# Kernel optimization log

Hardware: AMD Instinct MI355X
Metric: run time of the kernel (lower is better)

The kernel has to match this reference:

```python
import jax, jax.numpy as jnp
import numpy as np

TEMPERATURE = 0.1
B, D, A = 8192, 256, 4


def setup_inputs() -> dict:
    key = jax.random.key(0)
    k1, k2 = jax.random.split(key)
    # scale by 1/sqrt(D) so dot products are O(1) and exp(sim/T) is finite
    embeddings = jax.random.normal(k1, (B, D), dtype=jnp.float32) / jnp.sqrt(jnp.float32(D))
    labels = jax.random.randint(k2, (B, A), 0, 6, dtype=jnp.int64)
    return {"embeddings": embeddings, "labels": labels}


def reference(embeddings, labels):
    b = embeddings.shape[0]
    # [B, B] similarity scaled by temperature
    sim = jnp.matmul(embeddings, embeddings.T) / TEMPERATURE
    # positive mask: ANY aspect matches (vectorized over aspects), diagonal zeroed
    pos_mask = jnp.any(labels[:, None, :] == labels[None, :, :], axis=-1)
    pos_mask = pos_mask & ~jnp.eye(b, dtype=bool)
    pos_mask = pos_mask.astype(sim.dtype)

    exp_sim = jnp.exp(sim)
    positive_sim = jnp.sum(exp_sim * pos_mask, axis=1)            # [B]
    all_sim = jnp.sum(exp_sim, axis=1) - jnp.diagonal(exp_sim)   # [B]

    valid = positive_sim > 0
    pos_safe = jnp.where(valid, positive_sim, 1.0)
    all_safe = jnp.where(valid, all_sim, 1.0)
    row_loss = jnp.where(valid, -jnp.log(pos_safe / (all_safe + 1e-8)), 0.0)

    num_pos = jnp.sum(valid.astype(sim.dtype))
    loss = jnp.where(num_pos > 0, jnp.sum(row_loss) / jnp.maximum(num_pos, 1.0), 0.0)
    return loss
```

## Files before the change

### kernel.cpp

```cpp
#include <hip/hip_runtime.h>
#include <stdint.h>

typedef float f32x4 __attribute__((ext_vector_type(4)));
typedef float f32x2 __attribute__((ext_vector_type(2)));
typedef long lng2 __attribute__((ext_vector_type(2)));

#define B_TOTAL 8192
#define DDIM 256
#define BM 128
#define BN 64
#define NSPLIT 16
#define COLS_PER (B_TOTAL / NSPLIT)
#define ITERS (COLS_PER / BN)
#define NBLOCKS ((B_TOTAL / BM) * NSPLIT)
#define SCALE_HALF 3.79828546f
#define LN2F 0.6931471805599453f

__global__ __launch_bounds__(256) void prep_all(
    const float* __restrict__ E, const int* __restrict__ lab,
    unsigned char* __restrict__ EbA, unsigned char* __restrict__ Bf,
    unsigned int* __restrict__ plab, float* __restrict__ posAll) {
  const int t = blockIdx.x * 256 + threadIdx.x;
  const float4* s4 = (const float4*)E + (size_t)t * 2;
  float4 v0 = s4[0], v1 = s4[1];
  unsigned int d0 = (unsigned int)__builtin_amdgcn_cvt_pk_fp8_f32(
      v0.x * SCALE_HALF, v0.y * SCALE_HALF, 0, false);
  d0 = (unsigned int)__builtin_amdgcn_cvt_pk_fp8_f32(
      v0.z * SCALE_HALF, v0.w * SCALE_HALF, (int)d0, true);
  unsigned int d1 = (unsigned int)__builtin_amdgcn_cvt_pk_fp8_f32(
      v1.x * SCALE_HALF, v1.y * SCALE_HALF, 0, false);
  d1 = (unsigned int)__builtin_amdgcn_cvt_pk_fp8_f32(
      v1.z * SCALE_HALF, v1.w * SCALE_HALF, (int)d1, true);
  const unsigned long long v8 =
      (unsigned long long)d0 | ((unsigned long long)d1 << 32);
  const int row = t >> 5, j = t & 31;
  *(unsigned long long*)(EbA + (size_t)row * DDIM + ((j & 3) * 64 + (j >> 2) * 8)) = v8;
  const unsigned int boff = (unsigned int)(row >> 4) * 4096u +
                            (unsigned int)(j >> 3) * 1024u +
                            (unsigned int)(j & 3) * 256u +
                            (unsigned int)(row & 15) * 16u +
                            (unsigned int)((j >> 2) & 1) * 8u;
  *(unsigned long long*)(Bf + boff) = v8;
  if (t < B_TOTAL) {
    int4 l = ((const int4*)lab)[t];
    plab[t] = (1u << ((unsigned)l.x & 31u))
            | (1u << (((unsigned)l.y & 31u) + 6u))
            | (1u << (((unsigned)l.z & 31u) + 12u))
            | (1u << (((unsigned)l.w & 31u) + 18u));
  }
  if (t < 2 * B_TOTAL) posAll[t] = 0.0f;
}

template <int DIAG>
__device__ __forceinline__ void epi_n(
    const f32x4 (&acc)[2], int n, int colbase, int itBN, int l15,
    const unsigned int (&pi)[2][4], const int (&irow)[2][4],
    const unsigned int* __restrict__ plab_all,
    f32x2 (&pos2)[2][2], f32x2 (&all2)[2][2]) {
  const int j = colbase + n * 16 + l15;
  const unsigned int hj = plab_all[itBN + n * 16 + l15];
#pragma unroll
  for (int m = 0; m < 2; ++m) {
    float e[4];
#pragma unroll
    for (int q = 0; q < 4; ++q) {
      float v = __builtin_amdgcn_exp2f(acc[m][q]);
      if (DIAG) { if (j == irow[m][q]) v = 0.0f; }
      e[q] = v;
    }
    f32x2 p01 = { (pi[m][0] & hj) ? e[0] : 0.0f, (pi[m][1] & hj) ? e[1] : 0.0f };
    f32x2 p23 = { (pi[m][2] & hj) ? e[2] : 0.0f, (pi[m][3] & hj) ? e[3] : 0.0f };
    all2[m][0] += (f32x2){e[0], e[1]};
    all2[m][1] += (f32x2){e[2], e[3]};
    pos2[m][0] += p01;
    pos2[m][1] += p23;
  }
}

template <int DIAG>
__device__ __forceinline__ void iter_body(
    const unsigned char* __restrict__ Bf, int ctbase,
    const unsigned int* __restrict__ plab_all,
    const long (&afrag)[2][8], const unsigned int (&pi)[2][4],
    const int (&irow)[2][4], int colbase, int itBN, int l15, int lane,
    f32x2 (&pos2)[2][2], f32x2 (&all2)[2][2]) {
  auto loadB = [&](int n, lng2 (&b)[4]) {
    const unsigned char* p = Bf + (size_t)(ctbase + n) * 4096 + (unsigned)lane * 16u;
#pragma unroll
    for (int kw8 = 0; kw8 < 4; ++kw8) b[kw8] = *(const lng2*)(p + kw8 * 1024);
  };
  auto mfmaN = [&](const lng2 (&b)[4], f32x4 (&acc)[2]) {
    acc[0] = (f32x4){0.f, 0.f, 0.f, 0.f};
    acc[1] = (f32x4){0.f, 0.f, 0.f, 0.f};
#pragma unroll
    for (int kw8 = 0; kw8 < 4; ++kw8) {
      acc[0] = __builtin_amdgcn_mfma_f32_16x16x32_fp8_fp8(
          afrag[0][kw8 * 2], b[kw8][0], acc[0], 0, 0, 0);
      acc[1] = __builtin_amdgcn_mfma_f32_16x16x32_fp8_fp8(
          afrag[1][kw8 * 2], b[kw8][0], acc[1], 0, 0, 0);
      acc[0] = __builtin_amdgcn_mfma_f32_16x16x32_fp8_fp8(
          afrag[0][kw8 * 2 + 1], b[kw8][1], acc[0], 0, 0, 0);
      acc[1] = __builtin_amdgcn_mfma_f32_16x16x32_fp8_fp8(
          afrag[1][kw8 * 2 + 1], b[kw8][1], acc[1], 0, 0, 0);
    }
  };
  lng2 b0[4], b1[4], b2_[4], b3[4];
  f32x4 accA[2], accB[2];
  loadB(0, b0); loadB(1, b1);
  mfmaN(b0, accA); loadB(2, b2_);
  mfmaN(b1, accB);
  epi_n<DIAG>(accA, 0, colbase, itBN, l15, pi, irow, plab_all, pos2, all2);
  mfmaN(b2_, accA); loadB(3, b3);
  epi_n<DIAG>(accB, 1, colbase, itBN, l15, pi, irow, plab_all, pos2, all2);
  mfmaN(b3, accB);
  epi_n<DIAG>(accA, 2, colbase, itBN, l15, pi, irow, plab_all, pos2, all2);
  epi_n<DIAG>(accB, 3, colbase, itBN, l15, pi, irow, plab_all, pos2, all2);
}

__global__ __launch_bounds__(256, 2) void main_kernel(
    const unsigned char* __restrict__ EbA, const unsigned char* __restrict__ Bf,
    const unsigned int* __restrict__ plab,
    float* __restrict__ posArr, float* __restrict__ allArr) {
  __shared__ unsigned int plab_all[COLS_PER];
  const int tid = threadIdx.x;
  const int lane = tid & 63;
  const int wid = tid >> 6;
  const int l15 = lane & 15;
  const int l4 = lane >> 4;
  const int rb = (int)blockIdx.x & 63;
  const int cs = (int)blockIdx.x >> 6;
  const int rowbase = rb * BM;
  const int colstart = cs * COLS_PER;

  long afrag[2][8];
#pragma unroll
  for (int m = 0; m < 2; ++m) {
    const int row = rowbase + wid * 32 + m * 16 + l15;
    const unsigned char* rp = EbA + (size_t)row * DDIM + l4 * 64;
#pragma unroll
    for (int kw8 = 0; kw8 < 4; ++kw8) {
      lng2 t = *(const lng2*)(rp + kw8 * 16);
      afrag[m][kw8 * 2] = t[0];
      afrag[m][kw8 * 2 + 1] = t[1];
    }
  }

  plab_all[tid] = plab[colstart + tid];
  plab_all[tid + 256] = plab[colstart + 256 + tid];

  unsigned int pi[2][4];
  int irow[2][4];
#pragma unroll
  for (int m = 0; m < 2; ++m)
#pragma unroll
    for (int q = 0; q < 4; ++q) {
      const int i = rowbase + wid * 32 + m * 16 + l4 * 4 + q;
      irow[m][q] = i;
      pi[m][q] = plab[i];
    }
  __syncthreads();

  f32x2 pos2[2][2] = {};
  f32x2 all2[2][2] = {};

  for (int it = 0; it < ITERS; ++it) {
    const int colbase = colstart + it * BN;
    const int ctbase = colbase >> 4;
    const bool hasDiag = (colbase < rowbase + BM) && (rowbase < colbase + BN);
    if (hasDiag)
      iter_body<1>(Bf, ctbase, plab_all, afrag, pi, irow,
                   colbase, it * BN, l15, lane, pos2, all2);
    else
      iter_body<0>(Bf, ctbase, plab_all, afrag, pi, irow,
                   colbase, it * BN, l15, lane, pos2, all2);
  }

#pragma unroll
  for (int m = 0; m < 2; ++m)
#pragma unroll
    for (int q = 0; q < 4; ++q) {
      float p = pos2[m][q >> 1][q & 1], al = all2[m][q >> 1][q & 1];
      p += __shfl_xor(p, 1); p += __shfl_xor(p, 2);
      p += __shfl_xor(p, 4); p += __shfl_xor(p, 8);
      al += __shfl_xor(al, 1); al += __shfl_xor(al, 2);
      al += __shfl_xor(al, 4); al += __shfl_xor(al, 8);
      if (l15 == 0) {
        atomicAdd(&posArr[irow[m][q]], p);
        atomicAdd(&allArr[irow[m][q]], al);
      }
    }
}

__global__ __launch_bounds__(1024) void finalize_kernel(
    const float* __restrict__ posArr, const float* __restrict__ allArr,
    float* __restrict__ out) {
  float ls = 0.f, cnt = 0.f;
#pragma unroll
  for (int k = 0; k < B_TOTAL / 1024; ++k) {
    const int i = threadIdx.x + (k << 10);
    const float p = posArr[i];
    const float a = allArr[i];
    if (p > 0.f) {
      ls += (__builtin_amdgcn_logf(a + 1e-8f) - __builtin_amdgcn_logf(p)) * LN2F;
      cnt += 1.f;
    }
  }
#pragma unroll
  for (int msk = 1; msk < 64; msk <<= 1) {
    ls += __shfl_xor(ls, msk);
    cnt += __shfl_xor(cnt, msk);
  }
  __shared__ float sls[16], scnt[16];
  const int w = threadIdx.x >> 6;
  if ((threadIdx.x & 63) == 0) { sls[w] = ls; scnt[w] = cnt; }
  __syncthreads();
  if (threadIdx.x == 0) {
    float L = 0.f, C = 0.f;
    for (int i = 0; i < 16; ++i) { L += sls[i]; C += scnt[i]; }
    out[0] = (C > 0.f) ? L / fmaxf(C, 1.f) : 0.f;
  }
}

extern "C" void kernel_launch(void* const* d_in, const int* in_sizes, int n_in,
                              void* d_out, int out_size, void* d_ws, size_t ws_size,
                              hipStream_t stream) {
  const float* E = (const float*)d_in[0];
  const int* lab = (const int*)d_in[1];
  float* out = (float*)d_out;
  char* ws = (char*)d_ws;

  unsigned char* EbA = (unsigned char*)ws;
  unsigned char* Bf = (unsigned char*)(ws + 2u * 1024u * 1024u);
  unsigned int* plab = (unsigned int*)(ws + 4u * 1024u * 1024u);
  float* posArr = (float*)(ws + 4u * 1024u * 1024u + 32u * 1024u);
  float* allArr = posArr + B_TOTAL;

  prep_all<<<1024, 256, 0, stream>>>(E, lab, EbA, Bf, plab, posArr);
  main_kernel<<<NBLOCKS, 256, 0, stream>>>(EbA, Bf, plab, posArr, allArr);
  finalize_kernel<<<1, 1024, 0, stream>>>(posArr, allArr, out);
}
```

Baseline: 97.92 us.

## Exploit similarity symmetry by computing only upper-triangular tile pairs

Replaces the full row-block by column-split grid with one block per upper-triangular 128x128 tile pair, taken from a lookup table built in the prep kernel. Off-diagonal tiles feed their exp values into both row sums and column sums through column-wise shuffles and atomics, so the matrix is about halved in MFMA and exp work. The cost is many more global atomics per tile, since each column adds 128 atomic adds. Blocks are also smaller and shorter, which raises launch and setup overhead per tile.

```diff
diff --git a/kernel.cpp b/kernel.cpp
--- a/kernel.cpp
+++ b/kernel.cpp
@@ -7,19 +7,17 @@
 
 #define B_TOTAL 8192
 #define DDIM 256
-#define BM 128
-#define BN 64
-#define NSPLIT 16
-#define COLS_PER (B_TOTAL / NSPLIT)
-#define ITERS (COLS_PER / BN)
-#define NBLOCKS ((B_TOTAL / BM) * NSPLIT)
+#define TILE 128
+#define NTILE (B_TOTAL / TILE)
+#define NPAIRS (NTILE * (NTILE + 1) / 2)
 #define SCALE_HALF 3.79828546f
 #define LN2F 0.6931471805599453f
 
 __global__ __launch_bounds__(256) void prep_all(
     const float* __restrict__ E, const int* __restrict__ lab,
     unsigned char* __restrict__ EbA, unsigned char* __restrict__ Bf,
-    unsigned int* __restrict__ plab, float* __restrict__ posAll) {
+    unsigned int* __restrict__ plab, float* __restrict__ posAll,
+    unsigned int* __restrict__ lut) {
   const int t = blockIdx.x * 256 + threadIdx.x;
   const float4* s4 = (const float4*)E + (size_t)t * 2;
   float4 v0 = s4[0], v1 = s4[1];
@@ -49,23 +47,32 @@
             | (1u << (((unsigned)l.w & 31u) + 18u));
   }
   if (t < 2 * B_TOTAL) posAll[t] = 0.0f;
-}
-
-template <int DIAG>
+  if (t < NTILE * NTILE) {
+    const int I = t >> 6, J = t & 63;
+    if (J >= I) {
+      const int idx = I * NTILE - (I * (I - 1)) / 2 + (J - I);
+      lut[idx] = ((unsigned)I << 8) | (unsigned)J;
+    }
+  }
+}
+
+template <int DIAGT>
 __device__ __forceinline__ void epi_n(
-    const f32x4 (&acc)[2], int n, int colbase, int itBN, int l15,
+    const f32x4 (&acc)[2], int n, int colbase, int l15, int l4,
     const unsigned int (&pi)[2][4], const int (&irow)[2][4],
-    const unsigned int* __restrict__ plab_all,
-    f32x2 (&pos2)[2][2], f32x2 (&all2)[2][2]) {
+    const unsigned int* __restrict__ plab_col,
+    f32x2 (&pos2)[2][2], f32x2 (&all2)[2][2],
+    float* __restrict__ posArr, float* __restrict__ allArr) {
   const int j = colbase + n * 16 + l15;
-  const unsigned int hj = plab_all[itBN + n * 16 + l15];
+  const unsigned int hj = plab_col[n * 16 + l15];
+  float colp = 0.f, cola = 0.f;
 #pragma unroll
   for (int m = 0; m < 2; ++m) {
     float e[4];
 #pragma unroll
     for (int q = 0; q < 4; ++q) {
       float v = __builtin_amdgcn_exp2f(acc[m][q]);
-      if (DIAG) { if (j == irow[m][q]) v = 0.0f; }
+      if (DIAGT) { if (j == irow[m][q]) v = 0.0f; }
       e[q] = v;
     }
     f32x2 p01 = { (pi[m][0] & hj) ? e[0] : 0.0f, (pi[m][1] & hj) ? e[1] : 0.0f };
@@ -74,16 +81,29 @@
     all2[m][1] += (f32x2){e[2], e[3]};
     pos2[m][0] += p01;
     pos2[m][1] += p23;
-  }
-}
-
-template <int DIAG>
-__device__ __forceinline__ void iter_body(
+    if (!DIAGT) {
+      cola += (e[0] + e[1]) + (e[2] + e[3]);
+      colp += (p01[0] + p01[1]) + (p23[0] + p23[1]);
+    }
+  }
+  if (!DIAGT) {
+    colp += __shfl_xor(colp, 16); colp += __shfl_xor(colp, 32);
+    cola += __shfl_xor(cola, 16); cola += __shfl_xor(cola, 32);
+    if (l4 == 0) {
+      atomicAdd(&posArr[j], colp);
+      atomicAdd(&allArr[j], cola);
+    }
+  }
+}
+
+template <int DIAGT>
+__device__ __forceinline__ void tile_body(
     const unsigned char* __restrict__ Bf, int ctbase,
-    const unsigned int* __restrict__ plab_all,
+    const unsigned int* __restrict__ plab_col,
     const long (&afrag)[2][8], const unsigned int (&pi)[2][4],
-    const int (&irow)[2][4], int colbase, int itBN, int l15, int lane,
-    f32x2 (&pos2)[2][2], f32x2 (&all2)[2][2]) {
+    const int (&irow)[2][4], int colbase, int l15, int l4, int lane,
+    f32x2 (&pos2)[2][2], f32x2 (&all2)[2][2],
+    float* __restrict__ posArr, float* __restrict__ allArr) {
   auto loadB = [&](int n, lng2 (&b)[4]) {
     const unsigned char* p = Bf + (size_t)(ctbase + n) * 4096 + (unsigned)lane * 16u;
 #pragma unroll
@@ -104,33 +124,45 @@
           afrag[1][kw8 * 2 + 1], b[kw8][1], acc[1], 0, 0, 0);
     }
   };
-  lng2 b0[4], b1[4], b2_[4], b3[4];
+#define EPI(ACC, N) epi_n<DIAGT>(ACC, N, colbase, l15, l4, pi, irow, plab_col, \
+                                 pos2, all2, posArr, allArr)
+  lng2 b0[4], b1[4];
   f32x4 accA[2], accB[2];
   loadB(0, b0); loadB(1, b1);
-  mfmaN(b0, accA); loadB(2, b2_);
+  mfmaN(b0, accA); loadB(2, b0);
+  mfmaN(b1, accB); loadB(3, b1);
+  EPI(accA, 0);
+  mfmaN(b0, accA); loadB(4, b0);
+  EPI(accB, 1);
+  mfmaN(b1, accB); loadB(5, b1);
+  EPI(accA, 2);
+  mfmaN(b0, accA); loadB(6, b0);
+  EPI(accB, 3);
+  mfmaN(b1, accB); loadB(7, b1);
+  EPI(accA, 4);
+  mfmaN(b0, accA);
+  EPI(accB, 5);
   mfmaN(b1, accB);
-  epi_n<DIAG>(accA, 0, colbase, itBN, l15, pi, irow, plab_all, pos2, all2);
-  mfmaN(b2_, accA); loadB(3, b3);
-  epi_n<DIAG>(accB, 1, colbase, itBN, l15, pi, irow, plab_all, pos2, all2);
-  mfmaN(b3, accB);
-  epi_n<DIAG>(accA, 2, colbase, itBN, l15, pi, irow, plab_all, pos2, all2);
-  epi_n<DIAG>(accB, 3, colbase, itBN, l15, pi, irow, plab_all, pos2, all2);
+  EPI(accA, 6);
+  EPI(accB, 7);
+#undef EPI
 }
 
 __global__ __launch_bounds__(256, 2) void main_kernel(
     const unsigned char* __restrict__ EbA, const unsigned char* __restrict__ Bf,
-    const unsigned int* __restrict__ plab,
+    const unsigned int* __restrict__ plab, const unsigned int* __restrict__ lut,
     float* __restrict__ posArr, float* __restrict__ allArr) {
-  __shared__ unsigned int plab_all[COLS_PER];
+  __shared__ unsigned int plab_col[TILE];
   const int tid = threadIdx.x;
   const int lane = tid & 63;
   const int wid = tid >> 6;
   const int l15 = lane & 15;
   const int l4 = lane >> 4;
-  const int rb = (int)blockIdx.x & 63;
-  const int cs = (int)blockIdx.x >> 6;
-  const int rowbase = rb * BM;
-  const int colstart = cs * COLS_PER;
+  const unsigned int pair = lut[blockIdx.x];
+  const int I = (int)(pair >> 8), J = (int)(pair & 255u);
+  const int rowbase = I * TILE;
+  const int colbase = J * TILE;
+  const int ctbase = J * 8;
 
   long afrag[2][8];
 #pragma unroll
@@ -145,8 +177,7 @@
     }
   }
 
-  plab_all[tid] = plab[colstart + tid];
-  plab_all[tid + 256] = plab[colstart + 256 + tid];
+  if (tid < TILE) plab_col[tid] = plab[colbase + tid];
 
   unsigned int pi[2][4];
   int irow[2][4];
@@ -163,17 +194,12 @@
   f32x2 pos2[2][2] = {};
   f32x2 all2[2][2] = {};
 
-  for (int it = 0; it < ITERS; ++it) {
-    const int colbase = colstart + it * BN;
-    const int ctbase = colbase >> 4;
-    const bool hasDiag = (colbase < rowbase + BM) && (rowbase < colbase + BN);
-    if (hasDiag)
-      iter_body<1>(Bf, ctbase, plab_all, afrag, pi, irow,
-                   colbase, it * BN, l15, lane, pos2, all2);
-    else
-      iter_body<0>(Bf, ctbase, plab_all, afrag, pi, irow,
-                   colbase, it * BN, l15, lane, pos2, all2);
-  }
+  if (I == J)
+    tile_body<1>(Bf, ctbase, plab_col, afrag, pi, irow, colbase,
+                 l15, l4, lane, pos2, all2, posArr, allArr);
+  else
+    tile_body<0>(Bf, ctbase, plab_col, afrag, pi, irow, colbase,
+                 l15, l4, lane, pos2, all2, posArr, allArr);
 
 #pragma unroll
   for (int m = 0; m < 2; ++m)
@@ -234,8 +260,9 @@
   unsigned int* plab = (unsigned int*)(ws + 4u * 1024u * 1024u);
   float* posArr = (float*)(ws + 4u * 1024u * 1024u + 32u * 1024u);
   float* allArr = posArr + B_TOTAL;
-
-  prep_all<<<1024, 256, 0, stream>>>(E, lab, EbA, Bf, plab, posArr);
-  main_kernel<<<NBLOCKS, 256, 0, stream>>>(EbA, Bf, plab, posArr, allArr);
+  unsigned int* lut = (unsigned int*)(allArr + B_TOTAL);
+
+  prep_all<<<1024, 256, 0, stream>>>(E, lab, EbA, Bf, plab, posArr, lut);
+  main_kernel<<<NPAIRS, 256, 0, stream>>>(EbA, Bf, plab, lut, posArr, allArr);
   finalize_kernel<<<1, 1024, 0, stream>>>(posArr, allArr, out);
 }
```

New measurement: 124.1 us. +26.8%, slower.
